# Optimization experiments

Hardware: AMD Instinct MI355X
Metric: run time of the kernel (lower is better)

## Reference

```python
import jax, jax.numpy as jnp
import numpy as np

EPS = 1e-06

def _feature_map(x):
    # elu(x) + 1
    return jax.nn.elu(x) + 1.0

def setup_inputs() -> dict:
    key = jax.random.key(0)
    k1, k2, k3 = jax.random.split(key, 3)
    N, L, H, D = 4, 8192, 8, 128
    queries = jax.random.normal(k1, (N, L, H, D), dtype=jnp.float32)
    keys = jax.random.normal(k2, (N, L, H, D), dtype=jnp.float32)
    values = jax.random.normal(k3, (N, L, H, D), dtype=jnp.float32)
    threshold = jnp.array([0.1], dtype=jnp.float32)
    return {"queries": queries, "keys": keys, "values": values, "threshold": threshold}

def reference(queries, keys, values, threshold):
    Q = _feature_map(queries)            # [N,L,H,D]
    K = _feature_map(keys)               # [N,L,H,D]
    v_length = values.shape[1]
    v = values / v_length                # [N,L,H,V]
    KV = jnp.einsum('nshd,nshv->nhdv', K, v)            # [N,H,D,V]
    scores = jnp.einsum('nlhd,nhd->nlh', Q, K.sum(axis=1))  # [N,L,H]
    sparse = jnp.where(scores > threshold[0], scores, jnp.zeros_like(scores))
    Z = 1.0 / (sparse + EPS)             # [N,L,H]
    out = jnp.einsum('nlhd,nhdv,nlh->nlhv', Q, KV, Z) * v_length
    return out
```

## Files before the change

kernel.cpp:

```cpp
#include <hip/hip_runtime.h>
#include <stdint.h>


#define LSEQ 8192
#define NHD  1024
#define SP   20

typedef __attribute__((ext_vector_type(4))) float f32x4;
typedef __attribute__((ext_vector_type(8))) short bf16x8;
typedef unsigned short ushort_t;

static __device__ __forceinline__ unsigned short f2bf(float x) {
  union { float f; uint32_t u; } v; v.f = x;
  uint32_t r = v.u + 0x7FFFu + ((v.u >> 16) & 1u);
  return (unsigned short)(r >> 16);
}
static __device__ __forceinline__ uint32_t pack_bf(float a, float b) {
  return (uint32_t)f2bf(a) | ((uint32_t)f2bf(b) << 16);
}
static __device__ __forceinline__ float featmap(float x) {
  return x > 0.f ? x + 1.f : __expf(x);
}

#define BAR_LGKM() asm volatile("s_waitcnt lgkmcnt(0)\n\ts_barrier" ::: "memory")

__global__ __launch_bounds__(256, 4) void kv_vh(const float* __restrict__ keys,
                                                const float* __restrict__ values,
                                                float* __restrict__ kvp,
                                                float* __restrict__ kspart) {
  __shared__ uint32_t kls[128 * SP];
  __shared__ uint32_t vls[64 * SP];
  const int tid = threadIdx.x;
  const int chunk = blockIdx.x, CH = gridDim.x;
  const int h = blockIdx.y;
  const int n = blockIdx.z >> 1, vh = blockIdx.z & 1;
  const int nh = n * 8 + h;
  const int lane = tid & 63, w = tid >> 6;
  const int wr = w >> 1, wc = w & 1;
  const int lr = lane & 15, lg = lane >> 4;
  const int sPer = LSEQ / CH;
  const int steps = sPer / 32;

  const size_t gb = ((size_t)n * LSEQ + (size_t)chunk * sPer) * NHD + h * 128;
  const float* gk = keys + gb;
  const float* gv = values + gb + vh * 64;

  const int a = lane;
  const int fswA = 4 * ((a >> 2) & 3);
  const int kslot = (4 * w) ^ fswA;
  const int vloc = 2 * (a & 31);
  const int shalf = a >> 5;
  const int fswV = 4 * ((vloc >> 3) & 3);
  const int vslot = (4 * w + 2 * shalf) ^ fswV;

  f32x4 acc[4][2] = {};
  f32x4 ak[4] = {};
  bf16x8 ones;
  { uint32_t* u = (uint32_t*)&ones; u[0] = u[1] = u[2] = u[3] = 0x3F803F80u; }

#define ISSUE(T)                                                  \
  do {                                                            \
    _Pragma("unroll") for (int j = 0; j < 8; ++j)                 \
      kr[j] = *(const float2*)(gk + (size_t)((T) * 32 + 8 * w + j) * NHD + 2 * a); \
    _Pragma("unroll") for (int j = 0; j < 4; ++j)                 \
      vr[j] = *(const float2*)(gv + (size_t)((T) * 32 + 8 * w + 4 * shalf + j) * NHD + vloc); \
  } while (0)

  float2 kr[8], vr[4];
  ISSUE(0);

  for (int t = 0; t < steps; ++t) {
    {
      uint32_t k0[4], k1[4];
#pragma unroll
      for (int u = 0; u < 4; ++u) {
        k0[u] = pack_bf(featmap(kr[2 * u].x), featmap(kr[2 * u + 1].x));
        k1[u] = pack_bf(featmap(kr[2 * u].y), featmap(kr[2 * u + 1].y));
      }
      *(uint4*)&kls[(2 * a) * SP + kslot]     = make_uint4(k0[0], k0[1], k0[2], k0[3]);
      *(uint4*)&kls[(2 * a + 1) * SP + kslot] = make_uint4(k1[0], k1[1], k1[2], k1[3]);
      uint2 v0, v1;
      v0.x = pack_bf(vr[0].x, vr[1].x); v0.y = pack_bf(vr[2].x, vr[3].x);
      v1.x = pack_bf(vr[0].y, vr[1].y); v1.y = pack_bf(vr[2].y, vr[3].y);
      *(uint2*)&vls[vloc * SP + vslot]       = v0;
      *(uint2*)&vls[(vloc + 1) * SP + vslot] = v1;
    }
    BAR_LGKM();
    if (t + 1 < steps) ISSUE(t + 1);
    {
      bf16x8 af[4], bfr[2];
#pragma unroll
      for (int fr = 0; fr < 4; ++fr) {
        int d = wr * 64 + fr * 16 + lr;
        af[fr] = *(const bf16x8*)&kls[d * SP + ((4 * lg) ^ (4 * ((d >> 3) & 3)))];
      }
#pragma unroll
      for (int fc = 0; fc < 2; ++fc) {
        int v = wc * 32 + fc * 16 + lr;
        bfr[fc] = *(const bf16x8*)&vls[v * SP + ((4 * lg) ^ (4 * ((v >> 3) & 3)))];
      }
#pragma unroll
      for (int fr = 0; fr < 4; ++fr)
#pragma unroll
        for (int fc = 0; fc < 2; ++fc)
          acc[fr][fc] = __builtin_amdgcn_mfma_f32_16x16x32_bf16(af[fr], bfr[fc], acc[fr][fc], 0, 0, 0);
      if (wc == 0 && vh == 0) {
#pragma unroll
        for (int fr = 0; fr < 4; ++fr)
          ak[fr] = __builtin_amdgcn_mfma_f32_16x16x32_bf16(af[fr], ones, ak[fr], 0, 0, 0);
      }
    }
    BAR_LGKM();
  }
#undef ISSUE

  float* dst = kvp + ((size_t)chunk * 32 + nh) * 16384;
#pragma unroll
  for (int fr = 0; fr < 4; ++fr)
#pragma unroll
    for (int fc = 0; fc < 2; ++fc) {
      int d0 = wr * 64 + fr * 16 + lg * 4;
      int v  = vh * 64 + wc * 32 + fc * 16 + lr;
      *(float4*)(dst + (size_t)v * 128 + d0) =
          make_float4(acc[fr][fc][0], acc[fr][fc][1], acc[fr][fc][2], acc[fr][fc][3]);
    }
  if (wc == 0 && vh == 0 && lr == 0) {
    float* ks = kspart + ((size_t)chunk * 32 + nh) * 128;
#pragma unroll
    for (int fr = 0; fr < 4; ++fr)
      *(float4*)(ks + wr * 64 + fr * 16 + lg * 4) =
          make_float4(ak[fr][0], ak[fr][1], ak[fr][2], ak[fr][3]);
  }
}

__global__ __launch_bounds__(256) void kv_merge(const float* __restrict__ kvp,
                                                const float* __restrict__ kspart,
                                                ushort_t* __restrict__ kvb,
                                                float* __restrict__ ksumg,
                                                int CH) {
  const int nh = blockIdx.x, q = blockIdx.y, tid = threadIdx.x;
  const size_t off = (size_t)nh * 16384 + q * 4096;
#pragma unroll
  for (int i = 0; i < 4; ++i) {
    size_t idx = off + (size_t)(i * 256 + tid) * 4;
    f32x4 s = {};
    for (int c = 0; c < CH; ++c)
      s += *(const f32x4*)(kvp + (size_t)c * 524288 + idx);
    *(uint2*)(kvb + idx) = make_uint2(pack_bf(s[0], s[1]), pack_bf(s[2], s[3]));
  }
  if (q == 0 && tid < 128) {
    float s = 0.f;
    for (int c = 0; c < CH; ++c) s += kspart[((size_t)c * 32 + nh) * 128 + tid];
    ksumg[nh * 128 + tid] = s;
  }
}

__global__ __launch_bounds__(256, 4) void attn_out(const float* __restrict__ q,
                                                   const ushort_t* __restrict__ kvb,
                                                   const float* __restrict__ ksumg,
                                                   const float* __restrict__ thrp,
                                                   float* __restrict__ out) {
  __shared__ __align__(16) uint32_t As[128 * 17 * 4];
  __shared__ float zrow[128];

  const int tid = threadIdx.x;
  const int mc = blockIdx.x, nh = blockIdx.y;
  const int n = nh >> 3, h = nh & 7;
  const size_t qoff = ((size_t)(n * LSEQ + mc * 128)) * NHD + h * 128;
  const float thr = thrp[0];

  const int c4 = tid & 31;
  const float4 kk = *(const float4*)(ksumg + nh * 128 + c4 * 4);

#pragma unroll
  for (int it = 0; it < 16; ++it) {
    int rr = it * 8 + (tid >> 5);
    float4 qv = *(const float4*)(q + qoff + (size_t)rr * NHD + c4 * 4);
    float f0 = featmap(qv.x), f1 = featmap(qv.y), f2 = featmap(qv.z), f3 = featmap(qv.w);
    uint32_t* dst = &As[(rr * 17 + (c4 >> 1)) * 4 + (c4 & 1) * 2];
    dst[0] = pack_bf(f0, f1);
    dst[1] = pack_bf(f2, f3);
    float p = f0 * kk.x + f1 * kk.y + f2 * kk.z + f3 * kk.w;
    p += __shfl_xor(p, 1);  p += __shfl_xor(p, 2);  p += __shfl_xor(p, 4);
    p += __shfl_xor(p, 8);  p += __shfl_xor(p, 16);
    if (c4 == 0) {
      float sp = p > thr ? p : 0.f;
      zrow[rr] = 1.f / (sp + 1e-6f);
    }
  }
  __syncthreads();

  const int lane = tid & 63;
  const int w = tid >> 6;
  const int lr = lane & 15, lg = lane >> 4;
  const ushort_t* kvp = kvb + (size_t)nh * 16384;

  f32x4 acc0[8] = {};
  f32x4 acc1[8] = {};
#pragma unroll
  for (int ks = 0; ks < 4; ++ks) {
    const int c8 = ks * 4 + lg;
    const int dof = ks * 32 + lg * 8;
    const int r0 = w * 32 + lr;
    bf16x8 a0 = *(const bf16x8*)&As[(r0 * 17 + c8) * 4];
    bf16x8 a1 = *(const bf16x8*)&As[((r0 + 16) * 17 + c8) * 4];
#pragma unroll
    for (int ct = 0; ct < 8; ++ct) {
      bf16x8 bb = *(const bf16x8*)(kvp + (size_t)((ct * 16 + lr) * 128) + dof);
      acc0[ct] = __builtin_amdgcn_mfma_f32_16x16x32_bf16(a0, bb, acc0[ct], 0, 0, 0);
      acc1[ct] = __builtin_amdgcn_mfma_f32_16x16x32_bf16(a1, bb, acc1[ct], 0, 0, 0);
    }
  }

  float z0[4], z1[4];
#pragma unroll
  for (int j = 0; j < 4; ++j) {
    z0[j] = zrow[w * 32 + lg * 4 + j];
    z1[j] = zrow[w * 32 + 16 + lg * 4 + j];
  }
  float* op = out + qoff;
#pragma unroll
  for (int ct = 0; ct < 8; ++ct)
#pragma unroll
    for (int jj = 0; jj < 4; ++jj) {
      int row = w * 32 + lg * 4 + jj;
      op[(size_t)row * NHD + ct * 16 + lr]        = acc0[ct][jj] * z0[jj];
      op[(size_t)(row + 16) * NHD + ct * 16 + lr] = acc1[ct][jj] * z1[jj];
    }
}

extern "C" void kernel_launch(void* const* d_in, const int* in_sizes, int n_in,
                              void* d_out, int out_size, void* d_ws, size_t ws_size,
                              hipStream_t stream) {
  const float* queries   = (const float*)d_in[0];
  const float* keys      = (const float*)d_in[1];
  const float* values    = (const float*)d_in[2];
  const float* threshold = (const float*)d_in[3];
  float* out = (float*)d_out;

  int CH = 16;
  while (CH > 1 &&
         (size_t)CH * (524288 + 32 * 128) * 4 + (size_t)32 * 16384 * 2 + 32 * 128 * 4 > ws_size)
    CH >>= 1;
  float* kvp     = (float*)d_ws;
  float* kspart  = kvp + (size_t)CH * 524288;
  ushort_t* kvb  = (ushort_t*)(kspart + (size_t)CH * 32 * 128);
  float* ksumg   = (float*)(kvb + (size_t)32 * 16384);

  kv_vh<<<dim3(CH, 8, 8), 256, 0, stream>>>(keys, values, kvp, kspart);
  kv_merge<<<dim3(32, 4), 256, 0, stream>>>(kvp, kspart, kvb, ksumg, CH);
  attn_out<<<dim3(64, 32), 256, 0, stream>>>(queries, kvb, ksumg, threshold, out);
}
```

Before: 177.9 us.

## Compute full V width per block to avoid reloading and re-featurizing keys

The KV-partial kernel now uses 512-thread blocks that cover all 128 value columns, instead of two blocks each covering half of V. Previously each half re-read the keys and recomputed the feature map. Global loads become float4 per lane, and a cross-half lane shuffle transposes the data into the swizzled LDS layout. This halves key traffic and feature-map work, at the cost of larger blocks, extra shuffles and scalar LDS stores.

```diff
diff --git a/kernel.cpp b/kernel.cpp
--- a/kernel.cpp
+++ b/kernel.cpp
@@ -24,66 +24,74 @@
 
 #define BAR_LGKM() asm volatile("s_waitcnt lgkmcnt(0)\n\ts_barrier" ::: "memory")
 
-__global__ __launch_bounds__(256, 4) void kv_vh(const float* __restrict__ keys,
-                                                const float* __restrict__ values,
-                                                float* __restrict__ kvp,
-                                                float* __restrict__ kspart) {
+__global__ __launch_bounds__(512, 4) void kv_direct(const float* __restrict__ keys,
+                                                    const float* __restrict__ values,
+                                                    float* __restrict__ kvp,
+                                                    float* __restrict__ kspart) {
   __shared__ uint32_t kls[128 * SP];
-  __shared__ uint32_t vls[64 * SP];
+  __shared__ uint32_t vls[128 * SP];
   const int tid = threadIdx.x;
   const int chunk = blockIdx.x, CH = gridDim.x;
-  const int h = blockIdx.y;
-  const int n = blockIdx.z >> 1, vh = blockIdx.z & 1;
-  const int nh = n * 8 + h;
+  const int h = blockIdx.y, n = blockIdx.z, nh = n * 8 + h;
   const int lane = tid & 63, w = tid >> 6;
-  const int wr = w >> 1, wc = w & 1;
+  const int wr = w >> 2, wc = w & 3;
   const int lr = lane & 15, lg = lane >> 4;
   const int sPer = LSEQ / CH;
   const int steps = sPer / 32;
 
   const size_t gb = ((size_t)n * LSEQ + (size_t)chunk * sPer) * NHD + h * 128;
   const float* gk = keys + gb;
-  const float* gv = values + gb + vh * 64;
-
-  const int a = lane;
-  const int fswA = 4 * ((a >> 2) & 3);
-  const int kslot = (4 * w) ^ fswA;
-  const int vloc = 2 * (a & 31);
-  const int shalf = a >> 5;
-  const int fswV = 4 * ((vloc >> 3) & 3);
-  const int vslot = (4 * w + 2 * shalf) ^ fswV;
+  const float* gv = values + gb;
+
+  const int av = lane >> 5;
+  const int q  = lane & 31;
+  const int swzq = 4 * ((q >> 1) & 3);
+  const int base0 = (4 * q) * SP + ((2 * w + av) ^ swzq);
 
   f32x4 acc[4][2] = {};
   f32x4 ak[4] = {};
   bf16x8 ones;
   { uint32_t* u = (uint32_t*)&ones; u[0] = u[1] = u[2] = u[3] = 0x3F803F80u; }
 
-#define ISSUE(T)                                                  \
-  do {                                                            \
-    _Pragma("unroll") for (int j = 0; j < 8; ++j)                 \
-      kr[j] = *(const float2*)(gk + (size_t)((T) * 32 + 8 * w + j) * NHD + 2 * a); \
-    _Pragma("unroll") for (int j = 0; j < 4; ++j)                 \
-      vr[j] = *(const float2*)(gv + (size_t)((T) * 32 + 8 * w + 4 * shalf + j) * NHD + vloc); \
+#define ISSUE(T)                                                     \
+  do {                                                               \
+    _Pragma("unroll") for (int i = 0; i < 2; ++i) {                  \
+      size_t off = (size_t)((T) * 32 + 4 * w + av + 2 * i) * NHD + 4 * q; \
+      kr4[i] = *(const float4*)(gk + off);                           \
+      vr4[i] = *(const float4*)(gv + off);                           \
+    }                                                                \
   } while (0)
 
-  float2 kr[8], vr[4];
+  float4 kr4[2], vr4[2];
   ISSUE(0);
 
   for (int t = 0; t < steps; ++t) {
     {
-      uint32_t k0[4], k1[4];
-#pragma unroll
-      for (int u = 0; u < 4; ++u) {
-        k0[u] = pack_bf(featmap(kr[2 * u].x), featmap(kr[2 * u + 1].x));
-        k1[u] = pack_bf(featmap(kr[2 * u].y), featmap(kr[2 * u + 1].y));
-      }
-      *(uint4*)&kls[(2 * a) * SP + kslot]     = make_uint4(k0[0], k0[1], k0[2], k0[3]);
-      *(uint4*)&kls[(2 * a + 1) * SP + kslot] = make_uint4(k1[0], k1[1], k1[2], k1[3]);
-      uint2 v0, v1;
-      v0.x = pack_bf(vr[0].x, vr[1].x); v0.y = pack_bf(vr[2].x, vr[3].x);
-      v1.x = pack_bf(vr[0].y, vr[1].y); v1.y = pack_bf(vr[2].y, vr[3].y);
-      *(uint2*)&vls[vloc * SP + vslot]       = v0;
-      *(uint2*)&vls[(vloc + 1) * SP + vslot] = v1;
+      uint2 u0, u1, p0, p1, lo, hi;
+      u0.x = pack_bf(featmap(kr4[0].x), featmap(kr4[0].y));
+      u0.y = pack_bf(featmap(kr4[0].z), featmap(kr4[0].w));
+      u1.x = pack_bf(featmap(kr4[1].x), featmap(kr4[1].y));
+      u1.y = pack_bf(featmap(kr4[1].z), featmap(kr4[1].w));
+      p0.x = __shfl_xor((int)u0.x, 32); p0.y = __shfl_xor((int)u0.y, 32);
+      p1.x = __shfl_xor((int)u1.x, 32); p1.y = __shfl_xor((int)u1.y, 32);
+      lo.x = av ? p1.x : u0.x;  lo.y = av ? p1.y : u0.y;
+      hi.x = av ? u1.x : p0.x;  hi.y = av ? u1.y : p0.y;
+      kls[base0]          = (lo.x & 0xFFFFu) | (hi.x << 16);
+      kls[base0 + SP]     = (lo.x >> 16) | (hi.x & 0xFFFF0000u);
+      kls[base0 + 2 * SP] = (lo.y & 0xFFFFu) | (hi.y << 16);
+      kls[base0 + 3 * SP] = (lo.y >> 16) | (hi.y & 0xFFFF0000u);
+      u0.x = pack_bf(vr4[0].x, vr4[0].y);
+      u0.y = pack_bf(vr4[0].z, vr4[0].w);
+      u1.x = pack_bf(vr4[1].x, vr4[1].y);
+      u1.y = pack_bf(vr4[1].z, vr4[1].w);
+      p0.x = __shfl_xor((int)u0.x, 32); p0.y = __shfl_xor((int)u0.y, 32);
+      p1.x = __shfl_xor((int)u1.x, 32); p1.y = __shfl_xor((int)u1.y, 32);
+      lo.x = av ? p1.x : u0.x;  lo.y = av ? p1.y : u0.y;
+      hi.x = av ? u1.x : p0.x;  hi.y = av ? u1.y : p0.y;
+      vls[base0]          = (lo.x & 0xFFFFu) | (hi.x << 16);
+      vls[base0 + SP]     = (lo.x >> 16) | (hi.x & 0xFFFF0000u);
+      vls[base0 + 2 * SP] = (lo.y & 0xFFFFu) | (hi.y << 16);
+      vls[base0 + 3 * SP] = (lo.y >> 16) | (hi.y & 0xFFFF0000u);
     }
     BAR_LGKM();
     if (t + 1 < steps) ISSUE(t + 1);
@@ -104,7 +112,7 @@
 #pragma unroll
         for (int fc = 0; fc < 2; ++fc)
           acc[fr][fc] = __builtin_amdgcn_mfma_f32_16x16x32_bf16(af[fr], bfr[fc], acc[fr][fc], 0, 0, 0);
-      if (wc == 0 && vh == 0) {
+      if (wc == 0) {
 #pragma unroll
         for (int fr = 0; fr < 4; ++fr)
           ak[fr] = __builtin_amdgcn_mfma_f32_16x16x32_bf16(af[fr], ones, ak[fr], 0, 0, 0);
@@ -120,11 +128,11 @@
 #pragma unroll
     for (int fc = 0; fc < 2; ++fc) {
       int d0 = wr * 64 + fr * 16 + lg * 4;
-      int v  = vh * 64 + wc * 32 + fc * 16 + lr;
+      int v  = wc * 32 + fc * 16 + lr;
       *(float4*)(dst + (size_t)v * 128 + d0) =
           make_float4(acc[fr][fc][0], acc[fr][fc][1], acc[fr][fc][2], acc[fr][fc][3]);
     }
-  if (wc == 0 && vh == 0 && lr == 0) {
+  if (wc == 0 && lr == 0) {
     float* ks = kspart + ((size_t)chunk * 32 + nh) * 128;
 #pragma unroll
     for (int fr = 0; fr < 4; ++fr)
@@ -247,7 +255,7 @@
   ushort_t* kvb  = (ushort_t*)(kspart + (size_t)CH * 32 * 128);
   float* ksumg   = (float*)(kvb + (size_t)32 * 16384);
 
-  kv_vh<<<dim3(CH, 8, 8), 256, 0, stream>>>(keys, values, kvp, kspart);
+  kv_direct<<<dim3(CH, 8, 4), 512, 0, stream>>>(keys, values, kvp, kspart);
   kv_merge<<<dim3(32, 4), 256, 0, stream>>>(kvp, kspart, kvb, ksumg, CH);
   attn_out<<<dim3(64, 32), 256, 0, stream>>>(queries, kvb, ksumg, threshold, out);
 }
```

Measured after the change: 177.3 us. Within noise of the previous version (-0.4%).
